# Performance work log

Hardware: AMD Instinct MI355X
Metric: run time of the kernel (lower is better)

## Reference

```python
import jax, jax.numpy as jnp
import numpy as np

N, C = 4194304, 10
EPS = 1e-10
FOCAL_EPS = 1e-8
TEMP, THETA = 0.01, 0.1
NUM_TH = 21


def setup_inputs() -> dict:
    key = jax.random.key(0)
    k1, k2 = jax.random.split(key)
    logits = jax.random.normal(k1, (N, C), dtype=jnp.float32)
    probs = jax.nn.softmax(logits, axis=1)
    labels = jax.random.randint(k2, (N,), 0, C)
    y = jax.nn.one_hot(labels, C, dtype=jnp.float32)
    return {"probs": probs, "y": y}


def _soft_T(e):
    # sigmoid( (1/temp) * log( e*(1-theta) / clamp((1-e)*theta, eps) ) )
    num = e * (1.0 - THETA)
    den = jnp.maximum((1.0 - e) * THETA, EPS)
    frac = jnp.maximum(num / den, EPS)
    return jax.nn.sigmoid(jnp.log(frac) / TEMP)


def reference(probs, y):
    entmax = jnp.log(jnp.asarray(C, dtype=probs.dtype))
    predictions = jnp.argmax(probs, axis=1)             # [N]
    labels = jnp.argmax(y)                              # scalar (flattened argmax, as in torch code)

    # predictive uncertainty (type=0): entropy of probs per-sample
    unc = -jnp.sum(probs * jnp.log(jnp.maximum(probs, EPS)), axis=1)  # [N]

    th_list = jnp.linspace(0.0, 1.0, NUM_TH, dtype=probs.dtype)       # [21]
    umin, umax = jnp.min(unc), jnp.max(unc)
    unc_th = umin + th_list * (umax - umin)                           # [21]

    s = _soft_T(unc / entmax)                                         # [N]
    t = jnp.tanh(unc)                                                 # [N]
    w_cert = (1.0 - s) * (1.0 - t)   # weight when counted as 'certain'
    w_unc = s * t                    # weight when counted as 'uncertain'

    acc = (predictions == labels).astype(probs.dtype)                 # [N]
    inacc = 1.0 - acc

    le = (unc[None, :] <= unc_th[:, None]).astype(probs.dtype)        # [21, N]
    gt = 1.0 - le

    # one parallel masked-reduction pass over all 21 thresholds
    n_ac = le @ (acc * w_cert)
    n_au = gt @ (acc * w_unc)
    n_ic = le @ (inacc * w_cert)
    n_iu = gt @ (inacc * w_unc)

    avu = (n_ac + n_iu) / (n_ac + n_au + n_ic + n_iu + EPS)           # [21]

    # trapezoid rule over increasing th_list (direction = +1)
    dx = jnp.diff(th_list)
    auc_avu = jnp.sum((avu[1:] + avu[:-1]) * 0.5 * dx)

    # FocalLoss(gamma=1)
    logp = jnp.log(jnp.maximum(probs, FOCAL_EPS))
    ce_per = -jnp.sum(y * logp, axis=1)
    focal_per = -jnp.sum(y * logp * (1.0 - probs), axis=1)
    focal_loss = jnp.mean(focal_per)
    ce_loss = jnp.mean(ce_per)

    beta = 1.0
    savu_loss = -beta * jnp.log(jnp.maximum(auc_avu, EPS)) + focal_loss
    return (savu_loss, ce_loss)
```

## Files before the change

kernel.cpp:

```cpp
#include <hip/hip_runtime.h>

#define C 10
#define CHUNK_ROWS 128
#define CHUNK_FLOATS 1280
#define CHUNK_F4 320

__device__ __forceinline__ float waveSum(float v) {
#pragma unroll
  for (int o = 32; o > 0; o >>= 1) v += __shfl_down(v, o, 64);
  return v;
}
__device__ __forceinline__ float waveMin(float v) {
#pragma unroll
  for (int o = 32; o > 0; o >>= 1) v = fminf(v, __shfl_down(v, o, 64));
  return v;
}
__device__ __forceinline__ float waveMax(float v) {
#pragma unroll
  for (int o = 32; o > 0; o >>= 1) v = fmaxf(v, __shfl_down(v, o, 64));
  return v;
}
__device__ __forceinline__ unsigned waveMaxU(unsigned v) {
#pragma unroll
  for (int o = 32; o > 0; o >>= 1) {
    unsigned w = (unsigned)__shfl_down((int)v, o, 64);
    v = v > w ? v : w;
  }
  return v;
}

__global__ __launch_bounds__(128, 4) void pass1(
    const float4* __restrict__ probs4, const float4* __restrict__ y4,
    float2* __restrict__ us2,
    unsigned* __restrict__ uminInvSlots, unsigned* __restrict__ umaxSlots,
    float* __restrict__ ceSlots, float* __restrict__ focalSlots,
    int nchunks) {
  __shared__ float lds[2 * 2 * CHUNK_FLOATS];
  const int widx = threadIdx.x >> 6, lane = threadIdx.x & 63;
  float4* const bufP = (float4*)(lds + widx * (2 * CHUNK_FLOATS));
  float4* const bufS = bufP + CHUNK_F4;

  const int gw = blockIdx.x * 2 + widx;
  const int NW = gridDim.x * 2;

  int label0 = 0;
  {
    const float* yf = (const float*)y4;
    float m = yf[0];
#pragma unroll
    for (int c = 1; c < C; ++c) {
      float v = yf[c];
      if (v > m) { m = v; label0 = c; }
    }
  }

  float4 P[5], Y[5];
  auto issue = [&](int c) {
    const float4* gp = probs4 + (size_t)c * CHUNK_F4 + lane;
    const float4* gy = y4 + (size_t)c * CHUNK_F4 + lane;
#pragma unroll
    for (int q = 0; q < 5; ++q) { P[q] = gp[q * 64]; Y[q] = gy[q * 64]; }
  };

  float ceA = 0.f, foA = 0.f;
  float mnA = __uint_as_float(0x7f800000u), mxA = 0.f;

  if (gw < nchunks) issue(gw);
  for (int c = gw; c < nchunks; c += NW) {
#pragma unroll
    for (int q = 0; q < 5; ++q) {
      float4 pv = P[q], yv = Y[q];
      float lpx = __logf(fmaxf(pv.x, 1e-10f));
      float lpy = __logf(fmaxf(pv.y, 1e-10f));
      float lpz = __logf(fmaxf(pv.z, 1e-10f));
      float lpw = __logf(fmaxf(pv.w, 1e-10f));
      float4 sv = make_float4(pv.x * lpx, pv.y * lpy, pv.z * lpz, pv.w * lpw);
      float tx = yv.x * fmaxf(lpx, -18.420681f);
      float ty = yv.y * fmaxf(lpy, -18.420681f);
      float tz = yv.z * fmaxf(lpz, -18.420681f);
      float tw = yv.w * fmaxf(lpw, -18.420681f);
      ceA -= tx + ty + tz + tw;
      foA -= tx * (1.f - pv.x) + ty * (1.f - pv.y) + tz * (1.f - pv.z) +
             tw * (1.f - pv.w);
      bufP[q * 64 + lane] = pv;
      bufS[q * 64 + lane] = sv;
    }

    if (c + NW < nchunks) issue(c + NW);

    float R[20], S[20];
#pragma unroll
    for (int q = 0; q < 5; ++q) {
      float4 v = bufP[lane * 5 + q];
      R[4 * q] = v.x; R[4 * q + 1] = v.y; R[4 * q + 2] = v.z; R[4 * q + 3] = v.w;
      float4 w = bufS[lane * 5 + q];
      S[4 * q] = w.x; S[4 * q + 1] = w.y; S[4 * q + 2] = w.z; S[4 * q + 3] = w.w;
    }
    int am0 = 0, am1 = 0;
    float m0 = R[0], m1 = R[10];
#pragma unroll
    for (int cc = 1; cc < C; ++cc) {
      if (R[cc] > m0) { m0 = R[cc]; am0 = cc; }
      if (R[10 + cc] > m1) { m1 = R[10 + cc]; am1 = cc; }
    }
    float u0 = -(((S[0] + S[1]) + (S[2] + S[3])) + ((S[4] + S[5]) + (S[6] + S[7])) +
                 (S[8] + S[9]));
    float u1 = -(((S[10] + S[11]) + (S[12] + S[13])) +
                 ((S[14] + S[15]) + (S[16] + S[17])) + (S[18] + S[19]));
    mnA = fminf(mnA, fminf(u0, u1));
    mxA = fmaxf(mxA, fmaxf(u0, u1));

    unsigned s0 = __float_as_uint(u0) | ((am0 == label0) ? 0u : 0x80000000u);
    unsigned s1 = __float_as_uint(u1) | ((am1 == label0) ? 0u : 0x80000000u);
    us2[(size_t)c * 64 + lane] = make_float2(__uint_as_float(s0), __uint_as_float(s1));
  }

  float ce = waveSum(ceA), fo = waveSum(foA);
  float mn = waveMin(mnA), mx = waveMax(mxA);
  if (lane == 0) {
    int slot = gw & 63;
    atomicAdd(&ceSlots[slot], ce);
    atomicAdd(&focalSlots[slot], fo);
    atomicMax(&uminInvSlots[slot], ~__float_as_uint(mn));
    atomicMax(&umaxSlots[slot], __float_as_uint(mx));
  }
}

__global__ __launch_bounds__(256, 4) void pass2(
    const float4* __restrict__ us4, int n4,
    const unsigned* __restrict__ uminInvSlots, const unsigned* __restrict__ umaxSlots,
    float* __restrict__ ghist) {
  __shared__ float hist[88 * 64];
  __shared__ float smm[2];
  const int tid = threadIdx.x, lane = tid & 63;
  for (int i = tid; i < 88 * 64; i += 256) hist[i] = 0.f;
  if (tid < 64) {
    unsigned mnInv = waveMaxU(uminInvSlots[tid]);
    unsigned mxb = waveMaxU(umaxSlots[tid]);
    if (tid == 0) { smm[0] = __uint_as_float(~mnInv); smm[1] = __uint_as_float(mxb); }
  }
  __syncthreads();
  const float umin = smm[0], delta = smm[1] - smm[0];
  float th[21];
#pragma unroll
  for (int k = 0; k < 21; ++k) th[k] = fmaf(0.05f * (float)k, delta, umin);

  const int stride = gridDim.x * 256;
  for (int i = blockIdx.x * 256 + tid; i < n4; i += stride) {
    float4 v = us4[i];
    float vv[4] = {v.x, v.y, v.z, v.w};
#pragma unroll
    for (int q = 0; q < 4; ++q) {
      unsigned b = __float_as_uint(vv[q]);
      int rb = (b >> 31) ? 44 : 0;
      float u = __uint_as_float(b & 0x7fffffffu);
      float e = u * 0.4342944819f;
      float lnum = __logf(e * 0.9f);
      float lden = __logf(fmaxf((1.f - e) * 0.1f, 1e-10f));
      float x = fmaxf(lnum - lden, -23.0258509f) * 100.f;
      float s = __builtin_amdgcn_rcpf(1.f + __expf(-x));
      float t = 1.f - 2.f * __builtin_amdgcn_rcpf(__expf(2.f * u) + 1.f);
      float wc = (1.f - s) * (1.f - t), wu = s * t;
      int j = 0;
#pragma unroll
      for (int k = 0; k < 21; ++k) j += (u > th[k]) ? 1 : 0;
      atomicAdd(&hist[(rb + j) * 64 + lane], wc);
      atomicAdd(&hist[(rb + 22 + j) * 64 + lane], wu);
    }
  }
  __syncthreads();
#pragma unroll
  for (int st = 32; st >= 1; st >>= 1) {
    for (int idx = tid; idx < 88 * st; idx += 256) {
      int r = idx / st, c = idx - r * st;
      hist[r * 64 + c] += hist[r * 64 + c + st];
    }
    __syncthreads();
  }
  int slot = blockIdx.x & 63;
  for (int r = tid; r < 88; r += 256)
    atomicAdd(&ghist[slot * 88 + r], hist[r * 64]);
}

__global__ __launch_bounds__(256) void pass3(
    const float* __restrict__ ghist,
    const float* __restrict__ ceSlots, const float* __restrict__ focalSlots,
    float* __restrict__ out, float invN) {
  __shared__ float hr[88];
  __shared__ float scf[2];
  int tid = threadIdx.x;
  if (tid < 88) {
    float s = 0.f;
    for (int q = 0; q < 64; ++q) s += ghist[q * 88 + tid];
    hr[tid] = s;
  }
  if (tid >= 128 && tid < 192) {
    int l = tid - 128;
    float ce = waveSum(ceSlots[l]);
    float fo = waveSum(focalSlots[l]);
    if (l == 0) { scf[0] = ce; scf[1] = fo; }
  }
  __syncthreads();
  if (tid == 0) {
    float H0[22], H1[22], H2[22], H3[22];
    float totAU = 0.f, totIU = 0.f;
    for (int j = 0; j < 22; ++j) {
      H0[j] = hr[j]; H1[j] = hr[22 + j]; H2[j] = hr[44 + j]; H3[j] = hr[66 + j];
      totAU += H1[j]; totIU += H3[j];
    }
    float n_ac = 0.f, n_ic = 0.f, n_au = totAU, n_iu = totIU;
    float auc = 0.f, prev = 0.f;
    for (int k = 0; k < 21; ++k) {
      n_ac += H0[k]; n_ic += H2[k];
      n_au -= H1[k]; n_iu -= H3[k];
      float avu = (n_ac + n_iu) / (n_ac + n_au + n_ic + n_iu + 1e-10f);
      if (k > 0) auc += (avu + prev) * 0.5f * 0.05f;
      prev = avu;
    }
    out[0] = -logf(fmaxf(auc, 1e-10f)) + scf[1] * invN;
    out[1] = scf[0] * invN;
  }
}

extern "C" void kernel_launch(void* const* d_in, const int* in_sizes, int n_in,
                              void* d_out, int out_size, void* d_ws, size_t ws_size,
                              hipStream_t stream) {
  const float* probs = (const float*)d_in[0];
  const float* y = (const float*)d_in[1];
  float* out = (float*)d_out;
  const int N = in_sizes[0] / C;

  float* wsf = (float*)d_ws;
  unsigned* uminInvSlots = (unsigned*)wsf;
  unsigned* umaxSlots = (unsigned*)(wsf + 64);
  float* ceSlots = wsf + 128;
  float* focalSlots = wsf + 192;
  float* ghist = wsf + 256;
  float* us = wsf + 5888;

  hipMemsetAsync(d_ws, 0, 5888 * sizeof(float), stream);

  const int nchunks = N / CHUNK_ROWS;
  pass1<<<2048, 128, 0, stream>>>((const float4*)probs, (const float4*)y,
                                  (float2*)us, uminInvSlots, umaxSlots,
                                  ceSlots, focalSlots, nchunks);
  pass2<<<1024, 256, 0, stream>>>((const float4*)us, N / 4, uminInvSlots, umaxSlots,
                                  ghist);
  pass3<<<1, 256, 0, stream>>>(ghist, ceSlots, focalSlots, out, 1.0f / (float)N);
}
```

Baseline: 393.2 us.

## Fuse three passes into one cooperative kernel with grid syncs

Merges the three kernels into a single cooperative-launch kernel, using grid-wide syncs between the entropy/CE pass, the histogram pass and the final reduction, with the grid sized from occupancy. It also halves LDS use by recomputing the per-element logs in the transposed read instead of staging them, and narrows the histogram to 16 columns per row. The aim is to drop launch gaps and raise occupancy, at the cost of two grid barriers, redundant log work, and more LDS atomic contention.

Result: slower. 1.190 ms (+202.7%).

```diff
diff --git a/kernel.cpp b/kernel.cpp
--- a/kernel.cpp
+++ b/kernel.cpp
@@ -1,4 +1,7 @@
 #include <hip/hip_runtime.h>
+#include <hip/hip_cooperative_groups.h>
+
+namespace cg = cooperative_groups;
 
 #define C 10
 #define CHUNK_ROWS 128
@@ -29,204 +32,208 @@
   return v;
 }
 
-__global__ __launch_bounds__(128, 4) void pass1(
+__global__ __launch_bounds__(128, 8) void fused(
     const float4* __restrict__ probs4, const float4* __restrict__ y4,
     float2* __restrict__ us2,
     unsigned* __restrict__ uminInvSlots, unsigned* __restrict__ umaxSlots,
     float* __restrict__ ceSlots, float* __restrict__ focalSlots,
-    int nchunks) {
-  __shared__ float lds[2 * 2 * CHUNK_FLOATS];
-  const int widx = threadIdx.x >> 6, lane = threadIdx.x & 63;
-  float4* const bufP = (float4*)(lds + widx * (2 * CHUNK_FLOATS));
-  float4* const bufS = bufP + CHUNK_F4;
-
+    float* __restrict__ ghist, float* __restrict__ out,
+    int nchunks, float invN) {
+  __shared__ float lds[2560];
+  const int tid = threadIdx.x;
+  const int widx = tid >> 6, lane = tid & 63;
   const int gw = blockIdx.x * 2 + widx;
   const int NW = gridDim.x * 2;
 
-  int label0 = 0;
   {
-    const float* yf = (const float*)y4;
-    float m = yf[0];
-#pragma unroll
-    for (int c = 1; c < C; ++c) {
-      float v = yf[c];
-      if (v > m) { m = v; label0 = c; }
-    }
-  }
-
-  float4 P[5], Y[5];
-  auto issue = [&](int c) {
-    const float4* gp = probs4 + (size_t)c * CHUNK_F4 + lane;
-    const float4* gy = y4 + (size_t)c * CHUNK_F4 + lane;
-#pragma unroll
-    for (int q = 0; q < 5; ++q) { P[q] = gp[q * 64]; Y[q] = gy[q * 64]; }
-  };
-
-  float ceA = 0.f, foA = 0.f;
-  float mnA = __uint_as_float(0x7f800000u), mxA = 0.f;
-
-  if (gw < nchunks) issue(gw);
-  for (int c = gw; c < nchunks; c += NW) {
-#pragma unroll
-    for (int q = 0; q < 5; ++q) {
-      float4 pv = P[q], yv = Y[q];
-      float lpx = __logf(fmaxf(pv.x, 1e-10f));
-      float lpy = __logf(fmaxf(pv.y, 1e-10f));
-      float lpz = __logf(fmaxf(pv.z, 1e-10f));
-      float lpw = __logf(fmaxf(pv.w, 1e-10f));
-      float4 sv = make_float4(pv.x * lpx, pv.y * lpy, pv.z * lpz, pv.w * lpw);
-      float tx = yv.x * fmaxf(lpx, -18.420681f);
-      float ty = yv.y * fmaxf(lpy, -18.420681f);
-      float tz = yv.z * fmaxf(lpz, -18.420681f);
-      float tw = yv.w * fmaxf(lpw, -18.420681f);
-      ceA -= tx + ty + tz + tw;
-      foA -= tx * (1.f - pv.x) + ty * (1.f - pv.y) + tz * (1.f - pv.z) +
-             tw * (1.f - pv.w);
-      bufP[q * 64 + lane] = pv;
-      bufS[q * 64 + lane] = sv;
-    }
-
-    if (c + NW < nchunks) issue(c + NW);
-
-    float R[20], S[20];
-#pragma unroll
-    for (int q = 0; q < 5; ++q) {
-      float4 v = bufP[lane * 5 + q];
-      R[4 * q] = v.x; R[4 * q + 1] = v.y; R[4 * q + 2] = v.z; R[4 * q + 3] = v.w;
-      float4 w = bufS[lane * 5 + q];
-      S[4 * q] = w.x; S[4 * q + 1] = w.y; S[4 * q + 2] = w.z; S[4 * q + 3] = w.w;
-    }
-    int am0 = 0, am1 = 0;
-    float m0 = R[0], m1 = R[10];
-#pragma unroll
-    for (int cc = 1; cc < C; ++cc) {
-      if (R[cc] > m0) { m0 = R[cc]; am0 = cc; }
-      if (R[10 + cc] > m1) { m1 = R[10 + cc]; am1 = cc; }
-    }
-    float u0 = -(((S[0] + S[1]) + (S[2] + S[3])) + ((S[4] + S[5]) + (S[6] + S[7])) +
-                 (S[8] + S[9]));
-    float u1 = -(((S[10] + S[11]) + (S[12] + S[13])) +
-                 ((S[14] + S[15]) + (S[16] + S[17])) + (S[18] + S[19]));
-    mnA = fminf(mnA, fminf(u0, u1));
-    mxA = fmaxf(mxA, fmaxf(u0, u1));
-
-    unsigned s0 = __float_as_uint(u0) | ((am0 == label0) ? 0u : 0x80000000u);
-    unsigned s1 = __float_as_uint(u1) | ((am1 == label0) ? 0u : 0x80000000u);
-    us2[(size_t)c * 64 + lane] = make_float2(__uint_as_float(s0), __uint_as_float(s1));
-  }
-
-  float ce = waveSum(ceA), fo = waveSum(foA);
-  float mn = waveMin(mnA), mx = waveMax(mxA);
-  if (lane == 0) {
-    int slot = gw & 63;
-    atomicAdd(&ceSlots[slot], ce);
-    atomicAdd(&focalSlots[slot], fo);
-    atomicMax(&uminInvSlots[slot], ~__float_as_uint(mn));
-    atomicMax(&umaxSlots[slot], __float_as_uint(mx));
-  }
-}
-
-__global__ __launch_bounds__(256, 4) void pass2(
-    const float4* __restrict__ us4, int n4,
-    const unsigned* __restrict__ uminInvSlots, const unsigned* __restrict__ umaxSlots,
-    float* __restrict__ ghist) {
-  __shared__ float hist[88 * 64];
-  __shared__ float smm[2];
-  const int tid = threadIdx.x, lane = tid & 63;
-  for (int i = tid; i < 88 * 64; i += 256) hist[i] = 0.f;
-  if (tid < 64) {
-    unsigned mnInv = waveMaxU(uminInvSlots[tid]);
-    unsigned mxb = waveMaxU(umaxSlots[tid]);
-    if (tid == 0) { smm[0] = __uint_as_float(~mnInv); smm[1] = __uint_as_float(mxb); }
-  }
-  __syncthreads();
-  const float umin = smm[0], delta = smm[1] - smm[0];
-  float th[21];
-#pragma unroll
-  for (int k = 0; k < 21; ++k) th[k] = fmaf(0.05f * (float)k, delta, umin);
-
-  const int stride = gridDim.x * 256;
-  for (int i = blockIdx.x * 256 + tid; i < n4; i += stride) {
-    float4 v = us4[i];
-    float vv[4] = {v.x, v.y, v.z, v.w};
-#pragma unroll
-    for (int q = 0; q < 4; ++q) {
-      unsigned b = __float_as_uint(vv[q]);
-      int rb = (b >> 31) ? 44 : 0;
-      float u = __uint_as_float(b & 0x7fffffffu);
-      float e = u * 0.4342944819f;
-      float lnum = __logf(e * 0.9f);
-      float lden = __logf(fmaxf((1.f - e) * 0.1f, 1e-10f));
-      float x = fmaxf(lnum - lden, -23.0258509f) * 100.f;
-      float s = __builtin_amdgcn_rcpf(1.f + __expf(-x));
-      float t = 1.f - 2.f * __builtin_amdgcn_rcpf(__expf(2.f * u) + 1.f);
-      float wc = (1.f - s) * (1.f - t), wu = s * t;
-      int j = 0;
-#pragma unroll
-      for (int k = 0; k < 21; ++k) j += (u > th[k]) ? 1 : 0;
-      atomicAdd(&hist[(rb + j) * 64 + lane], wc);
-      atomicAdd(&hist[(rb + 22 + j) * 64 + lane], wu);
-    }
-  }
-  __syncthreads();
-#pragma unroll
-  for (int st = 32; st >= 1; st >>= 1) {
-    for (int idx = tid; idx < 88 * st; idx += 256) {
-      int r = idx / st, c = idx - r * st;
-      hist[r * 64 + c] += hist[r * 64 + c + st];
+    float4* const bufP = (float4*)(lds + widx * CHUNK_FLOATS);
+
+    int label0 = 0;
+    {
+      const float* yf = (const float*)y4;
+      float m = yf[0];
+#pragma unroll
+      for (int c = 1; c < C; ++c) {
+        float v = yf[c];
+        if (v > m) { m = v; label0 = c; }
+      }
+    }
+
+    float4 P[5], Y[5];
+    auto issue = [&](int c) {
+      const float4* gp = probs4 + (size_t)c * CHUNK_F4 + lane;
+      const float4* gy = y4 + (size_t)c * CHUNK_F4 + lane;
+#pragma unroll
+      for (int q = 0; q < 5; ++q) { P[q] = gp[q * 64]; Y[q] = gy[q * 64]; }
+    };
+
+    float ceA = 0.f, foA = 0.f;
+    float mnA = __uint_as_float(0x7f800000u), mxA = 0.f;
+
+    if (gw < nchunks) issue(gw);
+    for (int c = gw; c < nchunks; c += NW) {
+#pragma unroll
+      for (int q = 0; q < 5; ++q) {
+        float4 pv = P[q], yv = Y[q];
+        float lpx = __logf(fmaxf(pv.x, 1e-10f));
+        float lpy = __logf(fmaxf(pv.y, 1e-10f));
+        float lpz = __logf(fmaxf(pv.z, 1e-10f));
+        float lpw = __logf(fmaxf(pv.w, 1e-10f));
+        float tx = yv.x * fmaxf(lpx, -18.420681f);
+        float ty = yv.y * fmaxf(lpy, -18.420681f);
+        float tz = yv.z * fmaxf(lpz, -18.420681f);
+        float tw = yv.w * fmaxf(lpw, -18.420681f);
+        ceA -= tx + ty + tz + tw;
+        foA -= tx * (1.f - pv.x) + ty * (1.f - pv.y) + tz * (1.f - pv.z) +
+               tw * (1.f - pv.w);
+        bufP[q * 64 + lane] = pv;
+      }
+
+      if (c + NW < nchunks) issue(c + NW);
+
+      float u0 = 0.f, u1 = 0.f;
+      float m0 = -1.f, m1 = -1.f;
+      int am0 = 0, am1 = 0;
+#pragma unroll
+      for (int q = 0; q < 5; ++q) {
+        float4 v = bufP[lane * 5 + q];
+        float vv[4] = {v.x, v.y, v.z, v.w};
+#pragma unroll
+        for (int j = 0; j < 4; ++j) {
+          int e = 4 * q + j;
+          float p = vv[j];
+          float lp = __logf(fmaxf(p, 1e-10f));
+          if (e < 10) {
+            u0 -= p * lp;
+            if (p > m0) { m0 = p; am0 = e; }
+          } else {
+            u1 -= p * lp;
+            if (p > m1) { m1 = p; am1 = e - 10; }
+          }
+        }
+      }
+      mnA = fminf(mnA, fminf(u0, u1));
+      mxA = fmaxf(mxA, fmaxf(u0, u1));
+
+      unsigned s0 = __float_as_uint(u0) | ((am0 == label0) ? 0u : 0x80000000u);
+      unsigned s1 = __float_as_uint(u1) | ((am1 == label0) ? 0u : 0x80000000u);
+      us2[(size_t)c * 64 + lane] =
+          make_float2(__uint_as_float(s0), __uint_as_float(s1));
+    }
+
+    float ce = waveSum(ceA), fo = waveSum(foA);
+    float mn = waveMin(mnA), mx = waveMax(mxA);
+    if (lane == 0) {
+      int slot = gw & 63;
+      atomicAdd(&ceSlots[slot], ce);
+      atomicAdd(&focalSlots[slot], fo);
+      atomicMax(&uminInvSlots[slot], ~__float_as_uint(mn));
+      atomicMax(&umaxSlots[slot], __float_as_uint(mx));
+    }
+  }
+  __threadfence();
+  cg::this_grid().sync();
+
+  {
+    float* hist = lds;
+    float* smm = lds + 1408;
+    for (int i = tid; i < 1408; i += 128) hist[i] = 0.f;
+    if (tid < 64) {
+      unsigned mnInv = waveMaxU(uminInvSlots[tid]);
+      unsigned mxb = waveMaxU(umaxSlots[tid]);
+      if (tid == 0) {
+        smm[0] = __uint_as_float(~mnInv);
+        smm[1] = __uint_as_float(mxb);
+      }
     }
     __syncthreads();
-  }
-  int slot = blockIdx.x & 63;
-  for (int r = tid; r < 88; r += 256)
-    atomicAdd(&ghist[slot * 88 + r], hist[r * 64]);
-}
-
-__global__ __launch_bounds__(256) void pass3(
-    const float* __restrict__ ghist,
-    const float* __restrict__ ceSlots, const float* __restrict__ focalSlots,
-    float* __restrict__ out, float invN) {
-  __shared__ float hr[88];
-  __shared__ float scf[2];
-  int tid = threadIdx.x;
-  if (tid < 88) {
-    float s = 0.f;
-    for (int q = 0; q < 64; ++q) s += ghist[q * 88 + tid];
-    hr[tid] = s;
-  }
-  if (tid >= 128 && tid < 192) {
-    int l = tid - 128;
-    float ce = waveSum(ceSlots[l]);
-    float fo = waveSum(focalSlots[l]);
-    if (l == 0) { scf[0] = ce; scf[1] = fo; }
-  }
-  __syncthreads();
-  if (tid == 0) {
-    float H0[22], H1[22], H2[22], H3[22];
-    float totAU = 0.f, totIU = 0.f;
-    for (int j = 0; j < 22; ++j) {
-      H0[j] = hr[j]; H1[j] = hr[22 + j]; H2[j] = hr[44 + j]; H3[j] = hr[66 + j];
-      totAU += H1[j]; totIU += H3[j];
-    }
-    float n_ac = 0.f, n_ic = 0.f, n_au = totAU, n_iu = totIU;
-    float auc = 0.f, prev = 0.f;
-    for (int k = 0; k < 21; ++k) {
-      n_ac += H0[k]; n_ic += H2[k];
-      n_au -= H1[k]; n_iu -= H3[k];
-      float avu = (n_ac + n_iu) / (n_ac + n_au + n_ic + n_iu + 1e-10f);
-      if (k > 0) auc += (avu + prev) * 0.5f * 0.05f;
-      prev = avu;
-    }
-    out[0] = -logf(fmaxf(auc, 1e-10f)) + scf[1] * invN;
-    out[1] = scf[0] * invN;
+    const float umin = smm[0], delta = smm[1] - smm[0];
+    float th[21];
+#pragma unroll
+    for (int k = 0; k < 21; ++k) th[k] = fmaf(0.05f * (float)k, delta, umin);
+
+    const int col = lane & 15;
+    for (int c = gw; c < nchunks; c += NW) {
+      float2 v = us2[(size_t)c * 64 + lane];
+      float vv[2] = {v.x, v.y};
+#pragma unroll
+      for (int q = 0; q < 2; ++q) {
+        unsigned b = __float_as_uint(vv[q]);
+        int rb = (b >> 31) ? 44 : 0;
+        float u = __uint_as_float(b & 0x7fffffffu);
+        float e = u * 0.4342944819f;
+        float lnum = __logf(e * 0.9f);
+        float lden = __logf(fmaxf((1.f - e) * 0.1f, 1e-10f));
+        float x = fmaxf(lnum - lden, -23.0258509f) * 100.f;
+        float s = __builtin_amdgcn_rcpf(1.f + __expf(-x));
+        float t = 1.f - 2.f * __builtin_amdgcn_rcpf(__expf(2.f * u) + 1.f);
+        float wc = (1.f - s) * (1.f - t), wu = s * t;
+        int j = 0;
+#pragma unroll
+        for (int k = 0; k < 21; ++k) j += (u > th[k]) ? 1 : 0;
+        atomicAdd(&hist[(rb + j) * 16 + col], wc);
+        atomicAdd(&hist[(rb + 22 + j) * 16 + col], wu);
+      }
+    }
+    __syncthreads();
+#pragma unroll
+    for (int st = 8; st >= 1; st >>= 1) {
+      for (int idx = tid; idx < 88 * st; idx += 128) {
+        int r = idx / st, cc = idx - r * st;
+        hist[r * 16 + cc] += hist[r * 16 + cc + st];
+      }
+      __syncthreads();
+    }
+    int slot = blockIdx.x & 63;
+    for (int r = tid; r < 88; r += 128)
+      atomicAdd(&ghist[slot * 88 + r], hist[r * 16]);
+  }
+  __threadfence();
+  cg::this_grid().sync();
+
+  if (blockIdx.x == 0) {
+    float* hr = lds;
+    float* scf = lds + 88;
+    if (tid < 64) {
+      for (int r = tid; r < 88; r += 64) {
+        float s = 0.f;
+        for (int q = 0; q < 64; ++q) s += ghist[q * 88 + r];
+        hr[r] = s;
+      }
+    } else {
+      int l = tid - 64;
+      float ce = waveSum(ceSlots[l]);
+      float fo = waveSum(focalSlots[l]);
+      if (l == 0) { scf[0] = ce; scf[1] = fo; }
+    }
+    __syncthreads();
+    if (tid == 0) {
+      float H0[22], H1[22], H2[22], H3[22];
+      float totAU = 0.f, totIU = 0.f;
+      for (int j = 0; j < 22; ++j) {
+        H0[j] = hr[j]; H1[j] = hr[22 + j]; H2[j] = hr[44 + j]; H3[j] = hr[66 + j];
+        totAU += H1[j]; totIU += H3[j];
+      }
+      float n_ac = 0.f, n_ic = 0.f, n_au = totAU, n_iu = totIU;
+      float auc = 0.f, prev = 0.f;
+      for (int k = 0; k < 21; ++k) {
+        n_ac += H0[k]; n_ic += H2[k];
+        n_au -= H1[k]; n_iu -= H3[k];
+        float avu = (n_ac + n_iu) / (n_ac + n_au + n_ic + n_iu + 1e-10f);
+        if (k > 0) auc += (avu + prev) * 0.5f * 0.05f;
+        prev = avu;
+      }
+      out[0] = -logf(fmaxf(auc, 1e-10f)) + scf[1] * invN;
+      out[1] = scf[0] * invN;
+    }
   }
 }
 
 extern "C" void kernel_launch(void* const* d_in, const int* in_sizes, int n_in,
                               void* d_out, int out_size, void* d_ws, size_t ws_size,
                               hipStream_t stream) {
-  const float* probs = (const float*)d_in[0];
-  const float* y = (const float*)d_in[1];
+  const float4* probs4 = (const float4*)d_in[0];
+  const float4* y4 = (const float4*)d_in[1];
   float* out = (float*)d_out;
   const int N = in_sizes[0] / C;
 
@@ -236,15 +243,27 @@
   float* ceSlots = wsf + 128;
   float* focalSlots = wsf + 192;
   float* ghist = wsf + 256;
-  float* us = wsf + 5888;
+  float2* us2 = (float2*)(wsf + 5888);
 
   hipMemsetAsync(d_ws, 0, 5888 * sizeof(float), stream);
 
-  const int nchunks = N / CHUNK_ROWS;
-  pass1<<<2048, 128, 0, stream>>>((const float4*)probs, (const float4*)y,
-                                  (float2*)us, uminInvSlots, umaxSlots,
-                                  ceSlots, focalSlots, nchunks);
-  pass2<<<1024, 256, 0, stream>>>((const float4*)us, N / 4, uminInvSlots, umaxSlots,
-                                  ghist);
-  pass3<<<1, 256, 0, stream>>>(ghist, ceSlots, focalSlots, out, 1.0f / (float)N);
-}
+  int nchunks = N / CHUNK_ROWS;
+  float invN = 1.0f / (float)N;
+
+  static int grid = 0;
+  if (grid == 0) {
+    int maxb = 0, ncu = 0;
+    hipOccupancyMaxActiveBlocksPerMultiprocessor(&maxb, fused, 128, 0);
+    hipDeviceGetAttribute(&ncu, hipDeviceAttributeMultiprocessorCount, 0);
+    if (maxb < 1) maxb = 1;
+    if (ncu < 1) ncu = 256;
+    long g = (long)maxb * (long)ncu;
+    grid = (int)(g > 4096 ? 4096 : g);
+  }
+
+  void* args[] = {(void*)&probs4, (void*)&y4, (void*)&us2,
+                  (void*)&uminInvSlots, (void*)&umaxSlots,
+                  (void*)&ceSlots, (void*)&focalSlots,
+                  (void*)&ghist, (void*)&out, (void*)&nchunks, (void*)&invN};
+  hipLaunchCooperativeKernel(fused, dim3(grid), dim3(128), args, 0, stream);
+}
```

## Fuse final reduction into pass2 via last-block pattern, halve pass1 LDS

Applied to the files above, without the earlier changes.

The final scalar reduction kernel is folded into the histogram kernel. An atomic done-counter picks the last block, which sums the global histogram slots and writes the outputs, so one kernel launch goes away. pass1 no longer stores the p*log p values in LDS; each lane recomputes the log for its own rows after the transpose, which halves LDS per wave and raises possible occupancy. Grid sizes for pass1 and pass2 are doubled. The trade-offs are extra log work in pass1, threadfence/atomic overhead, and more atomic contention on the global slots.

New measurement: 513.2 us. 30.5% more time.

```diff
diff --git a/kernel.cpp b/kernel.cpp
--- a/kernel.cpp
+++ b/kernel.cpp
@@ -35,10 +35,9 @@
     unsigned* __restrict__ uminInvSlots, unsigned* __restrict__ umaxSlots,
     float* __restrict__ ceSlots, float* __restrict__ focalSlots,
     int nchunks) {
-  __shared__ float lds[2 * 2 * CHUNK_FLOATS];
+  __shared__ float lds[2 * CHUNK_FLOATS];
   const int widx = threadIdx.x >> 6, lane = threadIdx.x & 63;
-  float4* const bufP = (float4*)(lds + widx * (2 * CHUNK_FLOATS));
-  float4* const bufS = bufP + CHUNK_F4;
+  float4* const bufP = (float4*)(lds + widx * CHUNK_FLOATS);
 
   const int gw = blockIdx.x * 2 + widx;
   const int NW = gridDim.x * 2;
@@ -74,7 +73,6 @@
       float lpy = __logf(fmaxf(pv.y, 1e-10f));
       float lpz = __logf(fmaxf(pv.z, 1e-10f));
       float lpw = __logf(fmaxf(pv.w, 1e-10f));
-      float4 sv = make_float4(pv.x * lpx, pv.y * lpy, pv.z * lpz, pv.w * lpw);
       float tx = yv.x * fmaxf(lpx, -18.420681f);
       float ty = yv.y * fmaxf(lpy, -18.420681f);
       float tz = yv.z * fmaxf(lpz, -18.420681f);
@@ -83,36 +81,38 @@
       foA -= tx * (1.f - pv.x) + ty * (1.f - pv.y) + tz * (1.f - pv.z) +
              tw * (1.f - pv.w);
       bufP[q * 64 + lane] = pv;
-      bufS[q * 64 + lane] = sv;
     }
 
     if (c + NW < nchunks) issue(c + NW);
 
-    float R[20], S[20];
+    float u0 = 0.f, u1 = 0.f;
+    float m0 = -1.f, m1 = -1.f;
+    int am0 = 0, am1 = 0;
 #pragma unroll
     for (int q = 0; q < 5; ++q) {
       float4 v = bufP[lane * 5 + q];
-      R[4 * q] = v.x; R[4 * q + 1] = v.y; R[4 * q + 2] = v.z; R[4 * q + 3] = v.w;
-      float4 w = bufS[lane * 5 + q];
-      S[4 * q] = w.x; S[4 * q + 1] = w.y; S[4 * q + 2] = w.z; S[4 * q + 3] = w.w;
-    }
-    int am0 = 0, am1 = 0;
-    float m0 = R[0], m1 = R[10];
-#pragma unroll
-    for (int cc = 1; cc < C; ++cc) {
-      if (R[cc] > m0) { m0 = R[cc]; am0 = cc; }
-      if (R[10 + cc] > m1) { m1 = R[10 + cc]; am1 = cc; }
-    }
-    float u0 = -(((S[0] + S[1]) + (S[2] + S[3])) + ((S[4] + S[5]) + (S[6] + S[7])) +
-                 (S[8] + S[9]));
-    float u1 = -(((S[10] + S[11]) + (S[12] + S[13])) +
-                 ((S[14] + S[15]) + (S[16] + S[17])) + (S[18] + S[19]));
+      float vv[4] = {v.x, v.y, v.z, v.w};
+#pragma unroll
+      for (int j = 0; j < 4; ++j) {
+        int e = 4 * q + j;
+        float p = vv[j];
+        float lp = __logf(fmaxf(p, 1e-10f));
+        if (e < 10) {
+          u0 -= p * lp;
+          if (p > m0) { m0 = p; am0 = e; }
+        } else {
+          u1 -= p * lp;
+          if (p > m1) { m1 = p; am1 = e - 10; }
+        }
+      }
+    }
     mnA = fminf(mnA, fminf(u0, u1));
     mxA = fmaxf(mxA, fmaxf(u0, u1));
 
     unsigned s0 = __float_as_uint(u0) | ((am0 == label0) ? 0u : 0x80000000u);
     unsigned s1 = __float_as_uint(u1) | ((am1 == label0) ? 0u : 0x80000000u);
-    us2[(size_t)c * 64 + lane] = make_float2(__uint_as_float(s0), __uint_as_float(s1));
+    us2[(size_t)c * 64 + lane] =
+        make_float2(__uint_as_float(s0), __uint_as_float(s1));
   }
 
   float ce = waveSum(ceA), fo = waveSum(foA);
@@ -126,12 +126,15 @@
   }
 }
 
-__global__ __launch_bounds__(256, 4) void pass2(
+__global__ __launch_bounds__(256, 4) void pass2f(
     const float4* __restrict__ us4, int n4,
     const unsigned* __restrict__ uminInvSlots, const unsigned* __restrict__ umaxSlots,
-    float* __restrict__ ghist) {
+    const float* __restrict__ ceSlots, const float* __restrict__ focalSlots,
+    float* __restrict__ ghist, unsigned* __restrict__ doneCount,
+    float* __restrict__ out, float invN) {
   __shared__ float hist[88 * 64];
   __shared__ float smm[2];
+  __shared__ unsigned isLast;
   const int tid = threadIdx.x, lane = tid & 63;
   for (int i = tid; i < 88 * 64; i += 256) hist[i] = 0.f;
   if (tid < 64) {
@@ -180,18 +183,20 @@
   int slot = blockIdx.x & 63;
   for (int r = tid; r < 88; r += 256)
     atomicAdd(&ghist[slot * 88 + r], hist[r * 64]);
-}
-
-__global__ __launch_bounds__(256) void pass3(
-    const float* __restrict__ ghist,
-    const float* __restrict__ ceSlots, const float* __restrict__ focalSlots,
-    float* __restrict__ out, float invN) {
-  __shared__ float hr[88];
-  __shared__ float scf[2];
-  int tid = threadIdx.x;
+
+  __threadfence();
+  if (tid == 0) isLast = (atomicAdd(doneCount, 1u) == (unsigned)gridDim.x - 1u);
+  __syncthreads();
+  if (!isLast) return;
+  __threadfence();
+
+  float* hr = hist;
+  float* scf = hist + 96;
   if (tid < 88) {
     float s = 0.f;
-    for (int q = 0; q < 64; ++q) s += ghist[q * 88 + tid];
+    for (int q = 0; q < 64; ++q)
+      s += __hip_atomic_load(&ghist[q * 88 + tid], __ATOMIC_RELAXED,
+                             __HIP_MEMORY_SCOPE_AGENT);
     hr[tid] = s;
   }
   if (tid >= 128 && tid < 192) {
@@ -202,17 +207,13 @@
   }
   __syncthreads();
   if (tid == 0) {
-    float H0[22], H1[22], H2[22], H3[22];
     float totAU = 0.f, totIU = 0.f;
-    for (int j = 0; j < 22; ++j) {
-      H0[j] = hr[j]; H1[j] = hr[22 + j]; H2[j] = hr[44 + j]; H3[j] = hr[66 + j];
-      totAU += H1[j]; totIU += H3[j];
-    }
+    for (int j = 0; j < 22; ++j) { totAU += hr[22 + j]; totIU += hr[66 + j]; }
     float n_ac = 0.f, n_ic = 0.f, n_au = totAU, n_iu = totIU;
     float auc = 0.f, prev = 0.f;
     for (int k = 0; k < 21; ++k) {
-      n_ac += H0[k]; n_ic += H2[k];
-      n_au -= H1[k]; n_iu -= H3[k];
+      n_ac += hr[k]; n_ic += hr[44 + k];
+      n_au -= hr[22 + k]; n_iu -= hr[66 + k];
       float avu = (n_ac + n_iu) / (n_ac + n_au + n_ic + n_iu + 1e-10f);
       if (k > 0) auc += (avu + prev) * 0.5f * 0.05f;
       prev = avu;
@@ -235,16 +236,19 @@
   unsigned* umaxSlots = (unsigned*)(wsf + 64);
   float* ceSlots = wsf + 128;
   float* focalSlots = wsf + 192;
-  float* ghist = wsf + 256;
-  float* us = wsf + 5888;
-
-  hipMemsetAsync(d_ws, 0, 5888 * sizeof(float), stream);
+  unsigned* doneCount = (unsigned*)(wsf + 256);
+  float* ghist = wsf + 260;
+  float* us = wsf + 5892;
+
+  hipMemsetAsync(d_ws, 0, 5892 * sizeof(float), stream);
 
   const int nchunks = N / CHUNK_ROWS;
-  pass1<<<2048, 128, 0, stream>>>((const float4*)probs, (const float4*)y,
+  float invN = 1.0f / (float)N;
+
+  pass1<<<4096, 128, 0, stream>>>((const float4*)probs, (const float4*)y,
                                   (float2*)us, uminInvSlots, umaxSlots,
                                   ceSlots, focalSlots, nchunks);
-  pass2<<<1024, 256, 0, stream>>>((const float4*)us, N / 4, uminInvSlots, umaxSlots,
-                                  ghist);
-  pass3<<<1, 256, 0, stream>>>(ghist, ceSlots, focalSlots, out, 1.0f / (float)N);
-}
+  pass2f<<<2048, 256, 0, stream>>>((const float4*)us, N / 4, uminInvSlots,
+                                   umaxSlots, ceSlots, focalSlots, ghist,
+                                   doneCount, out, invN);
+}
```
